# Performance work log

Measured on AMD Instinct MI355X. Metric: run time of the kernel, lower is better.

## Reference

```python
import jax, jax.numpy as jnp
import numpy as np

EMBED = 1024
HEADS = 16
HEAD_DIM = EMBED // HEADS
B, S = 2, 2048


def setup_inputs() -> dict:
    key = jax.random.key(0)
    ks = jax.random.split(key, 9)
    std = 1.0 / np.sqrt(EMBED)
    def lin(k):
        kw, kb = jax.random.split(k)
        W = jax.random.uniform(kw, (EMBED, EMBED), jnp.float32, -std, std)
        b = jax.random.uniform(kb, (EMBED,), jnp.float32, -std, std)
        return W, b
    Wq, bq = lin(ks[0])
    Wk, bk = lin(ks[1])
    Wv, bv = lin(ks[2])
    Wo, bo = lin(ks[3])
    x = jax.random.normal(ks[4], (B, S, EMBED), jnp.float32)
    return {"x": x, "Wq": Wq, "bq": bq, "Wk": Wk, "bk": bk,
            "Wv": Wv, "bv": bv, "Wo": Wo, "bo": bo}


def reference(x, Wq, bq, Wk, bk, Wv, bv, Wo, bo):
    b, s, e = x.shape
    # projections (torch Linear: x @ W^T + b; here W stored as [in,out])
    Q = x @ Wq + bq
    K = x @ Wk + bk
    V = x @ Wv + bv
    # [b, h, s, d]
    Q = Q.reshape(b, s, HEADS, HEAD_DIM).transpose(0, 2, 1, 3)
    K = K.reshape(b, s, HEADS, HEAD_DIM).transpose(0, 2, 1, 3)
    V = V.reshape(b, s, HEADS, HEAD_DIM).transpose(0, 2, 1, 3)
    scores = jnp.einsum('bhqd,bhkd->bhqk', Q, K) / np.sqrt(HEAD_DIM)
    # causal mask: positions k > q masked to -inf
    causal = jnp.tril(jnp.ones((s, s), dtype=bool))
    scores = jnp.where(causal[None, None], scores, -jnp.inf)
    weights = jax.nn.softmax(scores, axis=-1)
    out = jnp.einsum('bhqk,bhkd->bhqd', weights, V)
    out = out.transpose(0, 2, 1, 3).reshape(b, s, e)
    return out @ Wo + bo
```

## Files before the change

kernel.cpp:

```cpp
#include <hip/hip_runtime.h>
#include <hip/hip_bf16.h>
#include <stdint.h>

#define EMBED 1024
#define HEADS 16
#define HDIM 64
#define BATCH 2
#define SEQ 2048
#define NROWS (BATCH*SEQ)

typedef __attribute__((ext_vector_type(8))) short short8;
typedef __attribute__((ext_vector_type(4))) float f32x4;
typedef __attribute__((ext_vector_type(2))) unsigned int uint2v;

#define LOG2E 1.44269504088896f

__device__ __forceinline__ unsigned short f2bf(float f) {
    __hip_bfloat16 b = __float2bfloat16(f);
    return *reinterpret_cast<unsigned short*>(&b);
}

__device__ __forceinline__ void g2l16(const void* g, void* l) {
    __builtin_amdgcn_global_load_lds(
        (const __attribute__((address_space(1))) unsigned int*)g,
        (__attribute__((address_space(3))) unsigned int*)l, 16, 0, 0);
}

__global__ void cast_x_kernel(const float* __restrict__ x,
                              unsigned short* __restrict__ xb, int n4) {
    int i = blockIdx.x * blockDim.x + threadIdx.x;
    if (i < n4) {
        float4 v = reinterpret_cast<const float4*>(x)[i];
        ushort4 o;
        o.x = f2bf(v.x); o.y = f2bf(v.y); o.z = f2bf(v.z); o.w = f2bf(v.w);
        reinterpret_cast<ushort4*>(xb)[i] = o;
    }
}

__global__ void transW_kernel(const float* __restrict__ W,
                              unsigned short* __restrict__ Wt) {
    __shared__ float tile[32][33];
    int tx = threadIdx.x, ty = threadIdx.y;
#pragma unroll
    for (int r = 0; r < 4; r++) {
        int i = blockIdx.y * 32 + ty + r * 8;
        int o = blockIdx.x * 32 + tx;
        tile[ty + r * 8][tx] = W[(size_t)i * EMBED + o];
    }
    __syncthreads();
    int i2 = blockIdx.y * 32 + tx;
#pragma unroll
    for (int r = 0; r < 4; r++) {
        int o2 = blockIdx.x * 32 + ty + r * 8;
        Wt[(size_t)o2 * EMBED + i2] = f2bf(tile[tx][ty + r * 8]);
    }
}

template<int MODE>
__global__ __launch_bounds__(256)
void gemm_kernel(const unsigned short* __restrict__ A,
                 const unsigned short* __restrict__ B,
                 int K,
                 unsigned short* __restrict__ Qo,
                 unsigned short* __restrict__ Ko,
                 unsigned short* __restrict__ Vto,
                 const float* __restrict__ bq,
                 const float* __restrict__ bk,
                 const float* __restrict__ bvv,
                 float* __restrict__ Co,
                 const float* __restrict__ bo) {
    __shared__ __attribute__((aligned(16))) unsigned short As[128 * 64];
    __shared__ __attribute__((aligned(16))) unsigned short Bs[128 * 64];
    const int t = threadIdx.x;
    const int lane = t & 63;
    const int w = t >> 6;
    const int wr = w >> 1, wc = w & 1;
    const int l15 = lane & 15, l16 = lane >> 4;
    const int m0 = blockIdx.y * 128;
    const int n0 = blockIdx.x * 128;

    f32x4 acc[4][4];
#pragma unroll
    for (int i = 0; i < 4; i++)
#pragma unroll
        for (int j = 0; j < 4; j++) acc[i][j] = (f32x4){0.f, 0.f, 0.f, 0.f};

    for (int k0 = 0; k0 < K; k0 += 64) {
        __syncthreads();
#pragma unroll
        for (int i = 0; i < 4; i++) {
            int c = i * 256 + t;
            int row = c >> 3;
            int lc = (c & 7) ^ (row & 7);
            g2l16(A + (size_t)(m0 + row) * K + k0 + lc * 8,
                  As + (size_t)(i * 256 + (t & ~63)) * 8);
        }
#pragma unroll
        for (int i = 0; i < 4; i++) {
            int c = i * 256 + t;
            int row = c >> 3;
            int lc = (c & 7) ^ (row & 7);
            g2l16(B + (size_t)(n0 + row) * K + k0 + lc * 8,
                  Bs + (size_t)(i * 256 + (t & ~63)) * 8);
        }
        __syncthreads();
#pragma unroll
        for (int kk = 0; kk < 2; kk++) {
            short8 a[4], b[4];
#pragma unroll
            for (int ai = 0; ai < 4; ai++) {
                int row = wr * 64 + ai * 16 + l15;
                int ch = kk * 4 + l16;
                a[ai] = *reinterpret_cast<const short8*>(
                    As + row * 64 + ((ch ^ (row & 7)) << 3));
            }
#pragma unroll
            for (int bj = 0; bj < 4; bj++) {
                int row = wc * 64 + bj * 16 + l15;
                int ch = kk * 4 + l16;
                b[bj] = *reinterpret_cast<const short8*>(
                    Bs + row * 64 + ((ch ^ (row & 7)) << 3));
            }
            __builtin_amdgcn_s_setprio(1);
#pragma unroll
            for (int ai = 0; ai < 4; ai++)
#pragma unroll
                for (int bj = 0; bj < 4; bj++)
                    acc[ai][bj] = __builtin_amdgcn_mfma_f32_16x16x32_bf16(
                        a[ai], b[bj], acc[ai][bj], 0, 0, 0);
            __builtin_amdgcn_s_setprio(0);
        }
    }

    if (MODE == 0) {
        const int which = n0 >> 10;
        const int coln = n0 & 1023;
        const float* bias = which == 0 ? bq : (which == 1 ? bk : bvv);
        const float scale = which == 0 ? 0.125f * LOG2E : 1.0f;
#pragma unroll
        for (int ai = 0; ai < 4; ai++) {
            int rowb = m0 + wr * 64 + ai * 16 + l16 * 4;
            int b_ = rowb >> 11;
            int s = rowb & 2047;
#pragma unroll
            for (int bj = 0; bj < 4; bj++) {
                int col = coln + wc * 64 + bj * 16 + l15;
                float bsv = bias[col];
                int h = col >> 6, d = col & 63;
                if (which < 2) {
                    unsigned short* dst = (which == 0) ? Qo : Ko;
                    size_t base = ((size_t)(b_ * HEADS + h)) * SEQ * HDIM;
#pragma unroll
                    for (int r = 0; r < 4; r++) {
                        float v = (acc[ai][bj][r] + bsv) * scale;
                        dst[base + (size_t)(s + r) * HDIM + d] = f2bf(v);
                    }
                } else {
                    ushort4 pk;
                    pk.x = f2bf(acc[ai][bj][0] + bsv);
                    pk.y = f2bf(acc[ai][bj][1] + bsv);
                    pk.z = f2bf(acc[ai][bj][2] + bsv);
                    pk.w = f2bf(acc[ai][bj][3] + bsv);
                    size_t off = ((size_t)(b_ * HEADS + h) * HDIM + d) * SEQ + s;
                    *reinterpret_cast<ushort4*>(Vto + off) = pk;
                }
            }
        }
    } else {
#pragma unroll
        for (int ai = 0; ai < 4; ai++) {
            int rowb = m0 + wr * 64 + ai * 16 + l16 * 4;
#pragma unroll
            for (int bj = 0; bj < 4; bj++) {
                int col = n0 + wc * 64 + bj * 16 + l15;
                float bsv = bo[col];
#pragma unroll
                for (int r = 0; r < 4; r++)
                    Co[(size_t)(rowb + r) * EMBED + col] = acc[ai][bj][r] + bsv;
            }
        }
    }
}

__device__ __forceinline__ void stage_kv(const unsigned short* __restrict__ Kg,
                                         const unsigned short* __restrict__ Vg,
                                         int kv0, unsigned short* Ksb,
                                         unsigned short* Vsb, int t) {
#pragma unroll
    for (int i = 0; i < 2; i++) {
        int c = i * 256 + t;
        int row = c >> 3;
        int lc = (c & 7) ^ (row & 7);
        g2l16(Kg + (size_t)(kv0 + row) * HDIM + lc * 8,
              Ksb + (i * 256 + (t & ~63)) * 8);
    }
#pragma unroll
    for (int i = 0; i < 2; i++) {
        int c = i * 256 + t;
        int d = c >> 3;
        int lc = (c & 7) ^ (d & 7);
        g2l16(Vg + (size_t)d * SEQ + kv0 + lc * 8,
              Vsb + (i * 256 + (t & ~63)) * 8);
    }
}

__global__ __launch_bounds__(256, 4)
void attn_kernel(const unsigned short* __restrict__ Q,
                 const unsigned short* __restrict__ Kk,
                 const unsigned short* __restrict__ Vt,
                 unsigned short* __restrict__ O) {
    __shared__ __attribute__((aligned(16))) unsigned short Ks[2][64 * 64];
    __shared__ __attribute__((aligned(16))) unsigned short Vs[2][64 * 64];
    __shared__ __attribute__((aligned(16))) unsigned short Ps[4][16 * 64];

    const int t = threadIdx.x;
    const int lane = t & 63;
    const int w = t >> 6;
    const int l15 = lane & 15, l16 = lane >> 4;

    const int id = blockIdx.x;
    const int xcd = id & 7;
    const int u = id >> 3;
    const int bh = xcd * 4 + (u & 3);
    const int su = u >> 2;
    const int qi = (su < 16) ? su : 47 - su;
    const int q0 = qi * 64;
    const size_t base = (size_t)bh * SEQ * HDIM;
    const unsigned short* Kg = Kk + base;
    const unsigned short* Vg = Vt + base;
    const int qrow0 = q0 + w * 16;

    short8 qf[2];
    {
        const unsigned short* Qg = Q + base + (size_t)qrow0 * HDIM;
#pragma unroll
        for (int kc = 0; kc < 2; kc++)
            qf[kc] = *reinterpret_cast<const short8*>(
                Qg + l15 * HDIM + (kc * 4 + l16) * 8);
    }

    f32x4 oacc[4];
#pragma unroll
    for (int nd = 0; nd < 4; nd++) oacc[nd] = (f32x4){0.f, 0.f, 0.f, 0.f};
    float m_run = -1e30f, l_run = 0.f;

    const int ntiles = qi + 1;

    stage_kv(Kg, Vg, 0, Ks[0], Vs[0], t);

    for (int tk = 0; tk < ntiles; tk++) {
        const int cur = tk & 1;
        asm volatile("s_waitcnt vmcnt(0)" ::: "memory");
        __builtin_amdgcn_s_barrier();
        asm volatile("" ::: "memory");
        if (tk + 1 < ntiles)
            stage_kv(Kg, Vg, (tk + 1) * 64, Ks[cur ^ 1], Vs[cur ^ 1], t);

        const unsigned short* Kb = Ks[cur];
        const unsigned short* Vb = Vs[cur];

        f32x4 sc[4];
#pragma unroll
        for (int kb = 0; kb < 4; kb++) sc[kb] = (f32x4){0.f, 0.f, 0.f, 0.f};
#pragma unroll
        for (int kc = 0; kc < 2; kc++) {
            short8 ka[4];
#pragma unroll
            for (int kb = 0; kb < 4; kb++) {
                int row = kb * 16 + l15;
                ka[kb] = *reinterpret_cast<const short8*>(
                    Kb + row * 64 + (((kc * 4 + l16) ^ (row & 7)) << 3));
            }
            __builtin_amdgcn_s_setprio(1);
#pragma unroll
            for (int kb = 0; kb < 4; kb++)
                sc[kb] = __builtin_amdgcn_mfma_f32_16x16x32_bf16(
                    ka[kb], qf[kc], sc[kb], 0, 0, 0);
            __builtin_amdgcn_s_setprio(0);
        }
        if (tk == ntiles - 1) {
            const int qloc = w * 16 + l15;
#pragma unroll
            for (int kb = 0; kb < 4; kb++)
#pragma unroll
                for (int r = 0; r < 4; r++) {
                    int kloc = kb * 16 + l16 * 4 + r;
                    sc[kb][r] = (kloc > qloc) ? -1e30f : sc[kb][r];
                }
        }
        float mx = -1e30f;
#pragma unroll
        for (int kb = 0; kb < 4; kb++)
            mx = fmaxf(mx, fmaxf(fmaxf(sc[kb][0], sc[kb][1]),
                                 fmaxf(sc[kb][2], sc[kb][3])));
        mx = fmaxf(mx, __shfl_xor(mx, 16));
        mx = fmaxf(mx, __shfl_xor(mx, 32));
        if (__any(mx > m_run + 8.0f)) {
            float mn = fmaxf(m_run, mx);
            float sf = __builtin_amdgcn_exp2f(m_run - mn);
            m_run = mn;
            l_run *= sf;
#pragma unroll
            for (int r = 0; r < 4; r++) {
                float sfr = __shfl(sf, l16 * 4 + r);
#pragma unroll
                for (int nd = 0; nd < 4; nd++) oacc[nd][r] *= sfr;
            }
        }
        {
            const int rx = (l15 & 7) << 3;
            float ps = 0.f;
#pragma unroll
            for (int kb = 0; kb < 4; kb++) {
                float p0 = __builtin_amdgcn_exp2f(sc[kb][0] - m_run);
                float p1 = __builtin_amdgcn_exp2f(sc[kb][1] - m_run);
                float p2 = __builtin_amdgcn_exp2f(sc[kb][2] - m_run);
                float p3 = __builtin_amdgcn_exp2f(sc[kb][3] - m_run);
                ps += (p0 + p1) + (p2 + p3);
                uint2v pk;
                pk.x = (unsigned int)f2bf(p0) | ((unsigned int)f2bf(p1) << 16);
                pk.y = (unsigned int)f2bf(p2) | ((unsigned int)f2bf(p3) << 16);
                int kel = (kb * 16 + l16 * 4) ^ rx;
                *reinterpret_cast<uint2v*>(&Ps[w][l15 * 64 + kel]) = pk;
            }
            ps += __shfl_xor(ps, 16);
            ps += __shfl_xor(ps, 32);
            l_run += ps;
        }
#pragma unroll
        for (int kc = 0; kc < 2; kc++) {
            short8 vb[4], pa;
#pragma unroll
            for (int nd = 0; nd < 4; nd++) {
                int row = nd * 16 + l15;
                vb[nd] = *reinterpret_cast<const short8*>(
                    Vb + row * 64 + (((kc * 4 + l16) ^ (row & 7)) << 3));
            }
            pa = *reinterpret_cast<const short8*>(
                &Ps[w][l15 * 64 + (((kc * 4 + l16) ^ (l15 & 7)) << 3)]);
            __builtin_amdgcn_s_setprio(1);
#pragma unroll
            for (int nd = 0; nd < 4; nd++)
                oacc[nd] = __builtin_amdgcn_mfma_f32_16x16x32_bf16(
                    pa, vb[nd], oacc[nd], 0, 0, 0);
            __builtin_amdgcn_s_setprio(0);
        }
    }

    const int b_ = bh >> 4, h = bh & 15;
    float li = 1.0f / l_run;
#pragma unroll
    for (int r = 0; r < 4; r++) {
        float lir = __shfl(li, l16 * 4 + r);
        int row = b_ * SEQ + qrow0 + l16 * 4 + r;
#pragma unroll
        for (int nd = 0; nd < 4; nd++)
            O[(size_t)row * EMBED + h * 64 + nd * 16 + l15] =
                f2bf(oacc[nd][r] * lir);
    }
}

extern "C" void kernel_launch(void* const* d_in, const int* in_sizes, int n_in,
                              void* d_out, int out_size, void* d_ws, size_t ws_size,
                              hipStream_t stream) {
    (void)in_sizes; (void)n_in; (void)out_size; (void)ws_size;
    const float* x  = (const float*)d_in[0];
    const float* Wq = (const float*)d_in[1];
    const float* bq = (const float*)d_in[2];
    const float* Wk = (const float*)d_in[3];
    const float* bk = (const float*)d_in[4];
    const float* Wv = (const float*)d_in[5];
    const float* bv = (const float*)d_in[6];
    const float* Wo = (const float*)d_in[7];
    const float* bo = (const float*)d_in[8];
    float* out = (float*)d_out;

    unsigned short* xb   = (unsigned short*)d_ws;
    unsigned short* Wqkv = xb + (size_t)NROWS * EMBED;
    unsigned short* Wot  = Wqkv + (size_t)3 * EMBED * EMBED;
    unsigned short* Qb   = Wot + (size_t)EMBED * EMBED;
    unsigned short* Kb   = Qb + (size_t)NROWS * EMBED;
    unsigned short* Vtb  = Kb + (size_t)NROWS * EMBED;
    unsigned short* attn = Vtb + (size_t)NROWS * EMBED;

    cast_x_kernel<<<(NROWS * EMBED / 4 + 255) / 256, 256, 0, stream>>>(
        x, xb, NROWS * EMBED / 4);
    dim3 tgrid(32, 32), tblk(32, 8);
    transW_kernel<<<tgrid, tblk, 0, stream>>>(Wq, Wqkv);
    transW_kernel<<<tgrid, tblk, 0, stream>>>(Wk, Wqkv + (size_t)EMBED * EMBED);
    transW_kernel<<<tgrid, tblk, 0, stream>>>(Wv, Wqkv + (size_t)2 * EMBED * EMBED);
    transW_kernel<<<tgrid, tblk, 0, stream>>>(Wo, Wot);

    gemm_kernel<0><<<dim3(24, 32), 256, 0, stream>>>(
        xb, Wqkv, EMBED, Qb, Kb, Vtb, bq, bk, bv, nullptr, nullptr);

    attn_kernel<<<1024, 256, 0, stream>>>(Qb, Kb, Vtb, attn);

    gemm_kernel<1><<<dim3(8, 32), 256, 0, stream>>>(
        attn, Wot, EMBED, nullptr, nullptr, nullptr, nullptr, nullptr, nullptr,
        out, bo);
}
```

Baseline: 113.1 us.

## Software-pipeline QK^T of the next KV tile with softmax/PV of the current tile

```diff
diff --git a/kernel.cpp b/kernel.cpp
--- a/kernel.cpp
+++ b/kernel.cpp
@@ -244,22 +244,9 @@
     for (int nd = 0; nd < 4; nd++) oacc[nd] = (f32x4){0.f, 0.f, 0.f, 0.f};
     float m_run = -1e30f, l_run = 0.f;
 
-    const int ntiles = qi + 1;
-
-    stage_kv(Kg, Vg, 0, Ks[0], Vs[0], t);
-
-    for (int tk = 0; tk < ntiles; tk++) {
-        const int cur = tk & 1;
-        asm volatile("s_waitcnt vmcnt(0)" ::: "memory");
-        __builtin_amdgcn_s_barrier();
-        asm volatile("" ::: "memory");
-        if (tk + 1 < ntiles)
-            stage_kv(Kg, Vg, (tk + 1) * 64, Ks[cur ^ 1], Vs[cur ^ 1], t);
-
-        const unsigned short* Kb = Ks[cur];
-        const unsigned short* Vb = Vs[cur];
-
-        f32x4 sc[4];
+    const int nt = qi + 1;
+
+    auto qkt = [&](f32x4 (&sc)[4], const unsigned short* Kb) {
 #pragma unroll
         for (int kb = 0; kb < 4; kb++) sc[kb] = (f32x4){0.f, 0.f, 0.f, 0.f};
 #pragma unroll
@@ -278,7 +265,10 @@
                     ka[kb], qf[kc], sc[kb], 0, 0, 0);
             __builtin_amdgcn_s_setprio(0);
         }
-        if (tk == ntiles - 1) {
+    };
+
+    auto softmax_pv = [&](f32x4 (&sc)[4], const unsigned short* Vb, bool diag) {
+        if (diag) {
             const int qloc = w * 16 + l15;
 #pragma unroll
             for (int kb = 0; kb < 4; kb++)
@@ -345,7 +335,38 @@
                     pa, vb[nd], oacc[nd], 0, 0, 0);
             __builtin_amdgcn_s_setprio(0);
         }
-    }
+    };
+
+    auto step = [&](f32x4 (&cur)[4], f32x4 (&nxt)[4], int tt) {
+        softmax_pv(cur, Vs[(tt - 1) & 1], false);
+        asm volatile("s_waitcnt vmcnt(0)" ::: "memory");
+        __builtin_amdgcn_s_barrier();
+        asm volatile("" ::: "memory");
+        if (tt + 1 < nt)
+            stage_kv(Kg, Vg, (tt + 1) * 64, Ks[(tt + 1) & 1], Vs[(tt + 1) & 1], t);
+        qkt(nxt, Ks[tt & 1]);
+    };
+
+    f32x4 scA[4], scB[4];
+
+    stage_kv(Kg, Vg, 0, Ks[0], Vs[0], t);
+    asm volatile("s_waitcnt vmcnt(0)" ::: "memory");
+    __builtin_amdgcn_s_barrier();
+    asm volatile("" ::: "memory");
+    if (nt > 1) stage_kv(Kg, Vg, 64, Ks[1], Vs[1], t);
+    qkt(scA, Ks[0]);
+
+    int tt = 1;
+    for (; tt + 1 < nt; tt += 2) {
+        step(scA, scB, tt);
+        step(scB, scA, tt + 1);
+    }
+    if (tt < nt) {
+        step(scA, scB, tt);
+#pragma unroll
+        for (int kb = 0; kb < 4; kb++) scA[kb] = scB[kb];
+    }
+    softmax_pv(scA, Vs[(nt - 1) & 1], true);
 
     const int b_ = bh >> 4, h = bh & 15;
     float li = 1.0f / l_run;
```

Result: no change. 111.3 us (-1.6%).
